# Kernel tuning notes

Hardware: AMD Instinct MI355X
Metric: run time of the kernel (lower is better)

## Reference

```python
import jax, jax.numpy as jnp
import numpy as np

B, L, C = 2, 2048, 1024
H, HD = 16, 64
MAX_SCALE_MUL = float(np.log(100.0))
SCALE = 1.0  # attn_l2_norm=True -> scale is 1


def setup_inputs() -> dict:
    key = jax.random.key(0)
    ks = jax.random.split(key, 6)
    x = jax.random.normal(ks[0], (B, L, C), dtype=jnp.float32)
    attn_bias = jax.random.normal(ks[1], (1, 1, L, L), dtype=jnp.float32)
    w_qkv = jax.random.normal(ks[2], (3 * C, C), dtype=jnp.float32) * (1.0 / np.sqrt(C))
    q_bias = jnp.zeros((C,), dtype=jnp.float32)
    v_bias = jnp.zeros((C,), dtype=jnp.float32)
    scale_mul = jnp.full((1, H, 1, 1), np.log(4.0), dtype=jnp.float32)  # scale_mul_1H11
    w_proj = jax.random.normal(ks[3], (C, C), dtype=jnp.float32) * (1.0 / np.sqrt(C))
    b_proj = jnp.zeros((C,), dtype=jnp.float32)
    return {"x": x, "attn_bias": attn_bias, "w_qkv": w_qkv, "q_bias": q_bias,
            "v_bias": v_bias, "scale_mul": scale_mul, "w_proj": w_proj, "b_proj": b_proj}


def reference(x, attn_bias, w_qkv, q_bias, v_bias, scale_mul, w_proj, b_proj):
    # qkv projection with concatenated bias (q_bias, zeros, v_bias)
    bias = jnp.concatenate([q_bias, jnp.zeros_like(q_bias), v_bias])  # [3C]
    qkv = jnp.einsum('blc,dc->bld', x, w_qkv) + bias                  # [B,L,3C]
    qkv = qkv.reshape(B, L, 3, H, HD).transpose(2, 0, 3, 1, 4)        # [3,B,H,L,HD]
    q, k, v = qkv[0], qkv[1], qkv[2]
    # attn_l2_norm path: L2-normalize q,k; q scaled by exp(clamped scale_mul)
    sm = jnp.exp(jnp.minimum(scale_mul, MAX_SCALE_MUL))               # [1,H,1,1]
    q = q / jnp.linalg.norm(q, axis=-1, keepdims=True) * sm
    k = k / jnp.linalg.norm(k, axis=-1, keepdims=True)
    # slow_attn: scaled scores + bias, softmax, weighted sum
    attn = jnp.einsum('bhld,bhmd->bhlm', q * SCALE, k) + attn_bias    # [B,H,L,L]
    p = jax.nn.softmax(attn, axis=-1)
    oup = jnp.einsum('bhlm,bhmd->bhld', p, v)                         # [B,H,L,HD]
    oup = oup.transpose(0, 2, 1, 3).reshape(B, L, C)
    return jnp.einsum('blc,dc->bld', oup, w_proj) + b_proj
```

## Files before the change

### kernel.cpp

```cpp
#include <hip/hip_runtime.h>
#include <cstdint>
#include <cstddef>
#include <math.h>

typedef __attribute__((ext_vector_type(8))) __bf16 bf16x8;
typedef __attribute__((ext_vector_type(4))) __bf16 bf16x4;
typedef __attribute__((ext_vector_type(4))) float f32x4;
typedef __attribute__((ext_vector_type(4))) unsigned int u32x4;

#define AS1 __attribute__((address_space(1)))
#define AS3 __attribute__((address_space(3)))

#define LOG2E 1.4426950408889634f

__device__ __forceinline__ void gld16(void* lds_uniform, const void* gaddr) {
  __builtin_amdgcn_global_load_lds((const AS1 unsigned int*)gaddr,
                                   (AS3 unsigned int*)lds_uniform, 16, 0, 0);
}

__global__ __launch_bounds__(256)
void prep_kernel(const float* __restrict__ x, const float* __restrict__ wqkv,
                 const float* __restrict__ wproj, const float* __restrict__ bias,
                 __bf16* __restrict__ xb, __bf16* __restrict__ wqkvb,
                 __bf16* __restrict__ wprojb, __bf16* __restrict__ btr) {
  __shared__ __bf16 T[32][264];
  const int b = blockIdx.x;
  const int tid = threadIdx.x;
  if (b < 8192) {
    const float* src; __bf16* dst; int off;
    if (b < 4096)      { src = x;     dst = xb;     off = b; }
    else if (b < 7168) { src = wqkv;  dst = wqkvb;  off = b - 4096; }
    else               { src = wproj; dst = wprojb; off = b - 7168; }
    const int i = (off * 256 + tid) * 4;
    const float4 v = *(const float4*)(src + i);
    bf16x4 o;
    o[0] = (__bf16)v.x; o[1] = (__bf16)v.y; o[2] = (__bf16)v.z; o[3] = (__bf16)v.w;
    *(bf16x4*)(dst + i) = o;
    return;
  }
  const int bb = b - 8192;
  const int rb = bb >> 3, cg = bb & 7;
  const float* src = bias + (size_t)(rb * 32) * 2048 + cg * 256;
#pragma unroll
  for (int i = 0; i < 8; ++i) {
    const int u = i * 256 + tid;
    const int r = u >> 6, c4 = (u & 63) * 4;
    const float4 v = *(const float4*)(src + (size_t)r * 2048 + c4);
    T[r][c4 + 0] = (__bf16)(v.x * LOG2E);
    T[r][c4 + 1] = (__bf16)(v.y * LOG2E);
    T[r][c4 + 2] = (__bf16)(v.z * LOG2E);
    T[r][c4 + 3] = (__bf16)(v.w * LOG2E);
  }
  __syncthreads();
  const int ktl = tid >> 6;
  const int lane = tid & 63, g = lane >> 4, cc = lane & 15;
#pragma unroll
  for (int sub = 0; sub < 2; ++sub) {
    __bf16 outv[16];
#pragma unroll
    for (int v = 0; v < 16; ++v) {
      const int ni = v >> 2, j = v & 3;
      outv[v] = T[sub * 16 + cc][ktl * 64 + ni * 16 + g * 4 + j];
    }
    __bf16* dst = btr + ((size_t)(((rb * 2 + sub) * 32) + cg * 4 + ktl) * 64 + lane) * 16;
    *(bf16x8*)(dst) = *(bf16x8*)(outv);
    *(bf16x8*)(dst + 8) = *(bf16x8*)(outv + 8);
  }
}

__global__ __launch_bounds__(256, 2)
void gemm_qkv_kernel(const __bf16* __restrict__ A, const __bf16* __restrict__ B,
                     const float* __restrict__ q_bias, const float* __restrict__ v_bias,
                     const float* __restrict__ scale_mul,
                     __bf16* __restrict__ qb, __bf16* __restrict__ ktp, __bf16* __restrict__ vb) {
  __shared__ __attribute__((aligned(16))) __bf16 As[2][128 * 32];
  __shared__ __attribute__((aligned(16))) __bf16 Bs[2][128 * 32];
  const int tid = threadIdx.x;
  const int w = tid >> 6, lane = tid & 63;
  const int bid = blockIdx.x;
  const int swz = (bid & 7) * 96 + (bid >> 3);
  const int m0 = (swz / 24) * 128, n0 = (swz % 24) * 128;
  const int wm = (w >> 1) * 64, wn = (w & 1) * 64;
  const int c = lane & 15, g = lane >> 4;
  f32x4 acc[4][4];
#pragma unroll
  for (int i = 0; i < 4; ++i)
#pragma unroll
    for (int j = 0; j < 4; ++j) acc[i][j] = (f32x4)(0.0f);

  const int r_row = lane >> 2;
  const int r_col = (lane & 3) * 16;
  const char* Abase = (const char*)A + (size_t)m0 * 2048;
  const char* Bbase = (const char*)B + (size_t)n0 * 2048;

  for (int kt = 0; kt < 1024; kt += 64) {
#pragma unroll
    for (int ks = 0; ks < 2; ++ks)
#pragma unroll
      for (int s = 0; s < 2; ++s) {
        const int R = w * 2 + s;
        const int row = R * 16 + r_row;
        gld16((char*)&As[ks][0] + R * 1024, Abase + (size_t)row * 2048 + kt * 2 + ks * 64 + r_col);
        gld16((char*)&Bs[ks][0] + R * 1024, Bbase + (size_t)row * 2048 + kt * 2 + ks * 64 + r_col);
      }
    __syncthreads();
#pragma unroll
    for (int ks = 0; ks < 2; ++ks) {
      bf16x8 af[4], bfr[4];
#pragma unroll
      for (int i = 0; i < 4; ++i) {
        af[i]  = *(const bf16x8*)((const char*)&As[ks][0] + (wm + i * 16 + c) * 64 + g * 16);
        bfr[i] = *(const bf16x8*)((const char*)&Bs[ks][0] + (wn + i * 16 + c) * 64 + g * 16);
      }
#pragma unroll
      for (int ni = 0; ni < 4; ++ni)
#pragma unroll
        for (int mi = 0; mi < 4; ++mi)
          acc[ni][mi] = __builtin_amdgcn_mfma_f32_16x16x32_bf16(bfr[ni], af[mi], acc[ni][mi], 0, 0, 0);
    }
    __syncthreads();
  }

  const int nbase = n0 + wn;
  const int which = nbase >> 10;
  const int h = (nbase >> 6) & 15;
  float smh = 1.0f;
  if (which == 0) smh = __expf(fminf(scale_mul[h], 4.605170185988091f)) * LOG2E;
  float4 cb[4];
#pragma unroll
  for (int ni = 0; ni < 4; ++ni) {
    if (which == 0)      cb[ni] = *(const float4*)(q_bias + nbase + ni * 16 + 4 * g);
    else if (which == 2) cb[ni] = *(const float4*)(v_bias + nbase - 2048 + ni * 16 + 4 * g);
    else                 cb[ni] = make_float4(0.f, 0.f, 0.f, 0.f);
  }
  const int mrow0 = m0 + wm;
  const int b2 = mrow0 >> 11;
  const int lpos0 = mrow0 & 2047;
  __bf16* kt_tile = ktp + (size_t)(b2 * 16 + h) * 131072 + (size_t)(lpos0 >> 6) * 4096;
  __bf16* dst_qv = ((which == 0) ? qb : vb) + ((size_t)((b2 * 16 + h) * 2048 + lpos0)) * 64;

#pragma unroll
  for (int mi = 0; mi < 4; ++mi) {
    float v[4][4];
    float ss = 0.0f;
#pragma unroll
    for (int ni = 0; ni < 4; ++ni) {
      v[ni][0] = acc[ni][mi][0] + cb[ni].x;
      v[ni][1] = acc[ni][mi][1] + cb[ni].y;
      v[ni][2] = acc[ni][mi][2] + cb[ni].z;
      v[ni][3] = acc[ni][mi][3] + cb[ni].w;
#pragma unroll
      for (int j = 0; j < 4; ++j) ss += v[ni][j] * v[ni][j];
    }
    ss += __shfl_xor(ss, 16, 64);
    ss += __shfl_xor(ss, 32, 64);
    const float sc = (which == 2) ? 1.0f : (rsqrtf(ss) * smh);
    const int key = mi * 16 + c;
    if (which == 1) {
#pragma unroll
      for (int ni = 0; ni < 4; ++ni) {
        bf16x4 pk;
        pk[0] = (__bf16)(v[ni][0] * sc); pk[1] = (__bf16)(v[ni][1] * sc);
        pk[2] = (__bf16)(v[ni][2] * sc); pk[3] = (__bf16)(v[ni][3] * sc);
        *(bf16x4*)(kt_tile + (ni >> 1) * 2048 + key * 32 + (ni & 1) * 16 + 4 * g) = pk;
      }
    } else {
      __bf16* drow = dst_qv + (size_t)key * 64;
#pragma unroll
      for (int ni = 0; ni < 4; ++ni) {
        bf16x4 pk;
        pk[0] = (__bf16)(v[ni][0] * sc); pk[1] = (__bf16)(v[ni][1] * sc);
        pk[2] = (__bf16)(v[ni][2] * sc); pk[3] = (__bf16)(v[ni][3] * sc);
        *(bf16x4*)(drow + ni * 16 + 4 * g) = pk;
      }
    }
  }
}

__global__ __launch_bounds__(256)
void vtrans_kernel(const __bf16* __restrict__ vb, __bf16* __restrict__ vtp) {
  __shared__ __attribute__((aligned(16))) __bf16 Vs[4][64 * 64];
  const int w = threadIdx.x >> 6, lane = threadIdx.x & 63;
  const int idx = blockIdx.x * 4 + w;
  const int bh = idx >> 5, tile = idx & 31;
  const __bf16* src = vb + ((size_t)bh * 2048 + tile * 64) * 64;
#pragma unroll
  for (int s = 0; s < 8; ++s)
    gld16((char*)&Vs[w][0] + s * 1024, (const char*)src + s * 1024 + lane * 16);
  __syncthreads();
  __bf16* outb = vtp + (size_t)idx * 4096;
  const int gg = lane & 3, cc = lane >> 2;
#pragma unroll
  for (int r = 0; r < 8; ++r) {
    const int o = r * 512 + lane * 8;
    const int ni = r & 3, ks = r >> 2;
    const int hd = ni * 16 + cc;
    const int key0 = ks * 32 + gg * 8;
    bf16x8 pk;
#pragma unroll
    for (int i = 0; i < 8; ++i)
      pk[i] = Vs[w][(key0 + i) * 64 + hd];
    *(bf16x8*)(outb + o) = pk;
  }
}

#define STAGE(t, b) {                                                          \
  const char* _ks = kp + (size_t)(t) * 8192 + w * 1024 + sl16;                 \
  const char* _vs = vp + (size_t)(t) * 8192 + w * 1024 + sl16;                 \
  gld16(&Kb[b][w * 1024], _ks);                                                \
  gld16(&Vb[b][w * 1024], _vs);                                                \
}

#define BAV(ni, j) ((ni * 4 + j < 8) ? bA0[(ni * 4 + j) & 7] : bA1[(ni * 4 + j) & 7])

#define COMPUTE(t, b) {                                                        \
  const char* _bb = bp + (size_t)(t) * 2048 + lane * 32;                       \
  bf16x8 bA0 = *(const bf16x8*)_bb;                                            \
  bf16x8 bA1 = *(const bf16x8*)(_bb + 16);                                     \
  bf16x8 kf[4][2];                                                             \
  _Pragma("unroll")                                                            \
  for (int ni = 0; ni < 4; ++ni)                                               \
    _Pragma("unroll")                                                          \
    for (int ks = 0; ks < 2; ++ks)                                             \
      kf[ni][ks] = *(const bf16x8*)(&Kb[b][0] + ks * 4096 + (ni * 16 + c) * 64 + gsw16); \
  f32x4 sacc[4];                                                               \
  __builtin_amdgcn_s_setprio(1);                                               \
  _Pragma("unroll")                                                            \
  for (int ni = 0; ni < 4; ++ni) {                                             \
    f32x4 s_ = __builtin_amdgcn_mfma_f32_16x16x32_bf16(kf[ni][0], qf[0], (f32x4)(0.0f), 0, 0, 0); \
    sacc[ni] = __builtin_amdgcn_mfma_f32_16x16x32_bf16(kf[ni][1], qf[1], s_, 0, 0, 0); \
  }                                                                            \
  __builtin_amdgcn_s_setprio(0);                                               \
  unsigned qp[4][2];                                                           \
  _Pragma("unroll")                                                            \
  for (int ni = 0; ni < 4; ++ni) {                                             \
    const float p0 = __builtin_amdgcn_exp2f(sacc[ni][0] + (float)BAV(ni, 0));  \
    const float p1 = __builtin_amdgcn_exp2f(sacc[ni][1] + (float)BAV(ni, 1));  \
    const float p2 = __builtin_amdgcn_exp2f(sacc[ni][2] + (float)BAV(ni, 2));  \
    const float p3 = __builtin_amdgcn_exp2f(sacc[ni][3] + (float)BAV(ni, 3));  \
    lsum += (p0 + p1) + (p2 + p3);                                             \
    asm("v_cvt_pk_bf16_f32 %0, %1, %2" : "=v"(qp[ni][0]) : "v"(p0), "v"(p1));  \
    asm("v_cvt_pk_bf16_f32 %0, %1, %2" : "=v"(qp[ni][1]) : "v"(p2), "v"(p3));  \
  }                                                                            \
  bf16x8 pf[2];                                                                \
  _Pragma("unroll")                                                            \
  for (int ks = 0; ks < 2; ++ks) {                                             \
    unsigned x0 = qp[2 * ks][0], x1 = qp[2 * ks][1];                           \
    unsigned y0 = qp[2 * ks + 1][0], y1 = qp[2 * ks + 1][1];                   \
    asm("v_permlane32_swap_b32 %0, %1" : "+v"(x0), "+v"(y0));                  \
    asm("v_permlane16_swap_b32 %0, %1" : "+v"(x0), "+v"(y0));                  \
    asm("v_permlane32_swap_b32 %0, %1" : "+v"(x1), "+v"(y1));                  \
    asm("v_permlane16_swap_b32 %0, %1" : "+v"(x1), "+v"(y1));                  \
    u32x4 t_; t_[0] = x0; t_[1] = x1; t_[2] = y0; t_[3] = y1;                  \
    pf[ks] = __builtin_bit_cast(bf16x8, t_);                                   \
  }                                                                            \
  __builtin_amdgcn_s_setprio(1);                                               \
  _Pragma("unroll")                                                            \
  for (int ni = 0; ni < 4; ++ni) {                                             \
    const bf16x8 v0 = *(const bf16x8*)(&Vb[b][0] + 0 * 4096 + ni * 1024 + c * 64 + gsw16); \
    const bf16x8 v1 = *(const bf16x8*)(&Vb[b][0] + 1 * 4096 + ni * 1024 + c * 64 + gsw16); \
    oacc[ni] = __builtin_amdgcn_mfma_f32_16x16x32_bf16(pf[0], v0, oacc[ni], 0, 0, 0); \
    oacc[ni] = __builtin_amdgcn_mfma_f32_16x16x32_bf16(pf[1], v1, oacc[ni], 0, 0, 0); \
  }                                                                            \
  __builtin_amdgcn_s_setprio(0);                                               \
}

__global__ __launch_bounds__(512, 4)
void attn_kernel(const __bf16* __restrict__ qb, const __bf16* __restrict__ ktp,
                 const __bf16* __restrict__ vtp, const __bf16* __restrict__ btr,
                 __bf16* __restrict__ oupb) {
  __shared__ __attribute__((aligned(16))) char Kb[2][8192];
  __shared__ __attribute__((aligned(16))) char Vb[2][8192];
  const int tid = threadIdx.x, w = tid >> 6, lane = tid & 63;
  const int c = lane & 15, g = lane >> 4;
  const int sl16 = (lane ^ ((lane >> 3) & 3)) * 16;
  const int gsw16 = (g ^ ((c >> 1) & 3)) * 16;
  const int idx = blockIdx.x;
  const int bh = idx & 31, rb = idx >> 5;
  const __bf16* qh = qb + (size_t)bh * (2048 * 64);
  const char* kp = (const char*)ktp + (size_t)bh * (32 * 8192);
  const char* vp = (const char*)vtp + (size_t)bh * (32 * 8192);
  const char* bp = (const char*)btr + (size_t)(rb * 8 + w) * 65536;
  const int q0 = rb * 128 + w * 16;
  const int b2 = bh >> 4, h = bh & 15;

  bf16x8 qf[2];
#pragma unroll
  for (int ks = 0; ks < 2; ++ks)
    qf[ks] = *(const bf16x8*)(qh + (size_t)(q0 + c) * 64 + ks * 32 + g * 8);

  f32x4 oacc[4];
  float lsum = 0.0f;
#pragma unroll
  for (int ni = 0; ni < 4; ++ni) oacc[ni] = (f32x4)(0.0f);

  STAGE(0, 0);
  __syncthreads();
#pragma unroll 1
  for (int tt = 0; tt < 32; tt += 2) {
    if (tt + 1 < 32) STAGE(tt + 1, 1);
    COMPUTE(tt, 0);
    __syncthreads();
    if (tt + 2 < 32) STAGE(tt + 2, 0);
    COMPUTE(tt + 1, 1);
    __syncthreads();
  }

  float l = lsum;
  l += __shfl_xor(l, 16, 64);
  l += __shfl_xor(l, 32, 64);
#pragma unroll
  for (int j = 0; j < 4; ++j) {
    const float lr = __shfl(l, g * 4 + j, 64);
    const float inv = 1.0f / lr;
    const int qrow = q0 + g * 4 + j;
    __bf16* orow = oupb + ((size_t)(b2 * 2048 + qrow) * 16 + h) * 64;
#pragma unroll
    for (int ni = 0; ni < 4; ++ni)
      orow[ni * 16 + c] = (__bf16)(oacc[ni][j] * inv);
  }
}

__global__ __launch_bounds__(256, 2)
void gemm_proj_kernel(const __bf16* __restrict__ A, const __bf16* __restrict__ B,
                      const float* __restrict__ b_proj, float* __restrict__ out) {
  __shared__ __attribute__((aligned(16))) __bf16 As[64 * 32];
  __shared__ __attribute__((aligned(16))) __bf16 Bs[128 * 32];
  const int tid = threadIdx.x;
  const int w = tid >> 6, lane = tid & 63;
  const int c = lane & 15, g = lane >> 4;
  const int m0 = blockIdx.y * 64, n0 = blockIdx.x * 128;
  const int wm = (w >> 1) * 32, wn = (w & 1) * 64;
  f32x4 acc[2][4];
#pragma unroll
  for (int i = 0; i < 2; ++i)
#pragma unroll
    for (int j = 0; j < 4; ++j) acc[i][j] = (f32x4)(0.0f);

  const int r_row = lane >> 2;
  const int r_col = (lane & 3) * 16;
  const char* Abase = (const char*)A + (size_t)m0 * 2048;
  const char* Bbase = (const char*)B + (size_t)n0 * 2048;

  for (int kt = 0; kt < 1024; kt += 32) {
    {
      const int row = w * 16 + r_row;
      gld16((char*)As + w * 1024, Abase + (size_t)row * 2048 + kt * 2 + r_col);
    }
#pragma unroll
    for (int s = 0; s < 2; ++s) {
      const int R = w * 2 + s;
      const int row = R * 16 + r_row;
      gld16((char*)Bs + R * 1024, Bbase + (size_t)row * 2048 + kt * 2 + r_col);
    }
    __syncthreads();
    bf16x8 af[2], bfr[4];
#pragma unroll
    for (int i = 0; i < 2; ++i)
      af[i] = *(const bf16x8*)((const char*)As + (wm + i * 16 + c) * 64 + g * 16);
#pragma unroll
    for (int i = 0; i < 4; ++i)
      bfr[i] = *(const bf16x8*)((const char*)Bs + (wn + i * 16 + c) * 64 + g * 16);
#pragma unroll
    for (int mi = 0; mi < 2; ++mi)
#pragma unroll
      for (int ni = 0; ni < 4; ++ni)
        acc[mi][ni] = __builtin_amdgcn_mfma_f32_16x16x32_bf16(af[mi], bfr[ni], acc[mi][ni], 0, 0, 0);
    __syncthreads();
  }

  float cbias[4];
#pragma unroll
  for (int ni = 0; ni < 4; ++ni) cbias[ni] = b_proj[n0 + wn + ni * 16 + c];
#pragma unroll
  for (int mi = 0; mi < 2; ++mi)
#pragma unroll
    for (int j = 0; j < 4; ++j) {
      const int m = m0 + wm + mi * 16 + g * 4 + j;
      float* orow = out + (size_t)m * 1024 + n0 + wn;
#pragma unroll
      for (int ni = 0; ni < 4; ++ni)
        orow[ni * 16 + c] = acc[mi][ni][j] + cbias[ni];
    }
}

extern "C" void kernel_launch(void* const* d_in, const int* in_sizes, int n_in,
                              void* d_out, int out_size, void* d_ws, size_t ws_size,
                              hipStream_t stream) {
  const float* x         = (const float*)d_in[0];
  const float* attn_bias = (const float*)d_in[1];
  const float* w_qkv     = (const float*)d_in[2];
  const float* q_bias    = (const float*)d_in[3];
  const float* v_bias    = (const float*)d_in[4];
  const float* scale_mul = (const float*)d_in[5];
  const float* w_proj    = (const float*)d_in[6];
  const float* b_proj    = (const float*)d_in[7];
  float* out = (float*)d_out;

  __bf16* xb     = (__bf16*)d_ws;
  __bf16* wqkvb  = xb + 4194304;
  __bf16* wprojb = wqkvb + 3145728;
  __bf16* qb     = wprojb + 1048576;
  __bf16* ktp    = qb + 4194304;
  __bf16* vtp    = ktp + 4194304;
  __bf16* btr    = vtp + 4194304;
  __bf16* vb     = btr + 4194304;
  __bf16* oupb   = xb;

  prep_kernel<<<8704, 256, 0, stream>>>(x, w_qkv, w_proj, attn_bias, xb, wqkvb, wprojb, btr);
  gemm_qkv_kernel<<<768, 256, 0, stream>>>(xb, wqkvb, q_bias, v_bias, scale_mul,
                                           qb, ktp, vb);
  vtrans_kernel<<<256, 256, 0, stream>>>(vb, vtp);
  attn_kernel<<<512, 512, 0, stream>>>(qb, ktp, vtp, btr, oupb);
  gemm_proj_kernel<<<dim3(8, 64), 256, 0, stream>>>(oupb, wprojb, b_proj, out);
}
```

Before: 212.8 us.

## Use 2-wave 128x64 warp tiles in QKV GEMM, deepen proj GEMM K-step

The QKV GEMM now runs 128 threads per block, and each wave computes a full 128x64 output strip with 32 accumulators instead of 64x64. Each B fragment is reused across 8 A fragments, which cuts LDS reads per MFMA. The K-tile layout of the epilogue is recomputed per row to match. The projection GEMM now loads two 32-wide K slices per barrier pair, halving the number of syncs. The trade-off is more register pressure and fewer waves per block in the QKV GEMM, which may reduce latency hiding.

```diff
diff --git a/kernel.cpp b/kernel.cpp
--- a/kernel.cpp
+++ b/kernel.cpp
@@ -68,7 +68,7 @@
   }
 }
 
-__global__ __launch_bounds__(256, 2)
+__global__ __launch_bounds__(128, 2)
 void gemm_qkv_kernel(const __bf16* __restrict__ A, const __bf16* __restrict__ B,
                      const float* __restrict__ q_bias, const float* __restrict__ v_bias,
                      const float* __restrict__ scale_mul,
@@ -80,13 +80,13 @@
   const int bid = blockIdx.x;
   const int swz = (bid & 7) * 96 + (bid >> 3);
   const int m0 = (swz / 24) * 128, n0 = (swz % 24) * 128;
-  const int wm = (w >> 1) * 64, wn = (w & 1) * 64;
+  const int wn = w * 64;
   const int c = lane & 15, g = lane >> 4;
-  f32x4 acc[4][4];
+  f32x4 acc[4][8];
 #pragma unroll
   for (int i = 0; i < 4; ++i)
 #pragma unroll
-    for (int j = 0; j < 4; ++j) acc[i][j] = (f32x4)(0.0f);
+    for (int j = 0; j < 8; ++j) acc[i][j] = (f32x4)(0.0f);
 
   const int r_row = lane >> 2;
   const int r_col = (lane & 3) * 16;
@@ -97,26 +97,26 @@
 #pragma unroll
     for (int ks = 0; ks < 2; ++ks)
 #pragma unroll
-      for (int s = 0; s < 2; ++s) {
-        const int R = w * 2 + s;
-        const int row = R * 16 + r_row;
-        gld16((char*)&As[ks][0] + R * 1024, Abase + (size_t)row * 2048 + kt * 2 + ks * 64 + r_col);
-        gld16((char*)&Bs[ks][0] + R * 1024, Bbase + (size_t)row * 2048 + kt * 2 + ks * 64 + r_col);
+      for (int r = 0; r < 4; ++r) {
+        const int chunk = r * 2 + w;
+        const int row = chunk * 16 + r_row;
+        gld16((char*)&As[ks][0] + chunk * 1024, Abase + (size_t)row * 2048 + kt * 2 + ks * 64 + r_col);
+        gld16((char*)&Bs[ks][0] + chunk * 1024, Bbase + (size_t)row * 2048 + kt * 2 + ks * 64 + r_col);
       }
     __syncthreads();
 #pragma unroll
     for (int ks = 0; ks < 2; ++ks) {
-      bf16x8 af[4], bfr[4];
-#pragma unroll
-      for (int i = 0; i < 4; ++i) {
-        af[i]  = *(const bf16x8*)((const char*)&As[ks][0] + (wm + i * 16 + c) * 64 + g * 16);
+      bf16x8 bfr[4];
+#pragma unroll
+      for (int i = 0; i < 4; ++i)
         bfr[i] = *(const bf16x8*)((const char*)&Bs[ks][0] + (wn + i * 16 + c) * 64 + g * 16);
-      }
-#pragma unroll
-      for (int ni = 0; ni < 4; ++ni)
-#pragma unroll
-        for (int mi = 0; mi < 4; ++mi)
-          acc[ni][mi] = __builtin_amdgcn_mfma_f32_16x16x32_bf16(bfr[ni], af[mi], acc[ni][mi], 0, 0, 0);
+#pragma unroll
+      for (int mi = 0; mi < 8; ++mi) {
+        const bf16x8 af = *(const bf16x8*)((const char*)&As[ks][0] + (mi * 16 + c) * 64 + g * 16);
+#pragma unroll
+        for (int ni = 0; ni < 4; ++ni)
+          acc[ni][mi] = __builtin_amdgcn_mfma_f32_16x16x32_bf16(bfr[ni], af, acc[ni][mi], 0, 0, 0);
+      }
     }
     __syncthreads();
   }
@@ -133,14 +133,13 @@
     else if (which == 2) cb[ni] = *(const float4*)(v_bias + nbase - 2048 + ni * 16 + 4 * g);
     else                 cb[ni] = make_float4(0.f, 0.f, 0.f, 0.f);
   }
-  const int mrow0 = m0 + wm;
-  const int b2 = mrow0 >> 11;
-  const int lpos0 = mrow0 & 2047;
-  __bf16* kt_tile = ktp + (size_t)(b2 * 16 + h) * 131072 + (size_t)(lpos0 >> 6) * 4096;
+  const int b2 = m0 >> 11;
+  const int lpos0 = m0 & 2047;
+  __bf16* kt_head = ktp + (size_t)(b2 * 16 + h) * 131072;
   __bf16* dst_qv = ((which == 0) ? qb : vb) + ((size_t)((b2 * 16 + h) * 2048 + lpos0)) * 64;
 
 #pragma unroll
-  for (int mi = 0; mi < 4; ++mi) {
+  for (int mi = 0; mi < 8; ++mi) {
     float v[4][4];
     float ss = 0.0f;
 #pragma unroll
@@ -157,12 +156,15 @@
     const float sc = (which == 2) ? 1.0f : (rsqrtf(ss) * smh);
     const int key = mi * 16 + c;
     if (which == 1) {
+      const int lpos = lpos0 + key;
+      __bf16* kt_tile = kt_head + (size_t)(lpos >> 6) * 4096;
+      const int k64 = lpos & 63;
 #pragma unroll
       for (int ni = 0; ni < 4; ++ni) {
         bf16x4 pk;
         pk[0] = (__bf16)(v[ni][0] * sc); pk[1] = (__bf16)(v[ni][1] * sc);
         pk[2] = (__bf16)(v[ni][2] * sc); pk[3] = (__bf16)(v[ni][3] * sc);
-        *(bf16x4*)(kt_tile + (ni >> 1) * 2048 + key * 32 + (ni & 1) * 16 + 4 * g) = pk;
+        *(bf16x4*)(kt_tile + (ni >> 1) * 2048 + k64 * 32 + (ni & 1) * 16 + 4 * g) = pk;
       }
     } else {
       __bf16* drow = dst_qv + (size_t)key * 64;
@@ -324,8 +326,8 @@
 __global__ __launch_bounds__(256, 2)
 void gemm_proj_kernel(const __bf16* __restrict__ A, const __bf16* __restrict__ B,
                       const float* __restrict__ b_proj, float* __restrict__ out) {
-  __shared__ __attribute__((aligned(16))) __bf16 As[64 * 32];
-  __shared__ __attribute__((aligned(16))) __bf16 Bs[128 * 32];
+  __shared__ __attribute__((aligned(16))) __bf16 As[2][64 * 32];
+  __shared__ __attribute__((aligned(16))) __bf16 Bs[2][128 * 32];
   const int tid = threadIdx.x;
   const int w = tid >> 6, lane = tid & 63;
   const int c = lane & 15, g = lane >> 4;
@@ -342,30 +344,36 @@
   const char* Abase = (const char*)A + (size_t)m0 * 2048;
   const char* Bbase = (const char*)B + (size_t)n0 * 2048;
 
-  for (int kt = 0; kt < 1024; kt += 32) {
-    {
-      const int row = w * 16 + r_row;
-      gld16((char*)As + w * 1024, Abase + (size_t)row * 2048 + kt * 2 + r_col);
-    }
-#pragma unroll
-    for (int s = 0; s < 2; ++s) {
-      const int R = w * 2 + s;
-      const int row = R * 16 + r_row;
-      gld16((char*)Bs + R * 1024, Bbase + (size_t)row * 2048 + kt * 2 + r_col);
-    }
-    __syncthreads();
-    bf16x8 af[2], bfr[4];
-#pragma unroll
-    for (int i = 0; i < 2; ++i)
-      af[i] = *(const bf16x8*)((const char*)As + (wm + i * 16 + c) * 64 + g * 16);
-#pragma unroll
-    for (int i = 0; i < 4; ++i)
-      bfr[i] = *(const bf16x8*)((const char*)Bs + (wn + i * 16 + c) * 64 + g * 16);
-#pragma unroll
-    for (int mi = 0; mi < 2; ++mi)
-#pragma unroll
-      for (int ni = 0; ni < 4; ++ni)
-        acc[mi][ni] = __builtin_amdgcn_mfma_f32_16x16x32_bf16(af[mi], bfr[ni], acc[mi][ni], 0, 0, 0);
+  for (int kt = 0; kt < 1024; kt += 64) {
+#pragma unroll
+    for (int ks = 0; ks < 2; ++ks) {
+      {
+        const int row = w * 16 + r_row;
+        gld16((char*)&As[ks][0] + w * 1024, Abase + (size_t)row * 2048 + kt * 2 + ks * 64 + r_col);
+      }
+#pragma unroll
+      for (int s = 0; s < 2; ++s) {
+        const int R = w * 2 + s;
+        const int row = R * 16 + r_row;
+        gld16((char*)&Bs[ks][0] + R * 1024, Bbase + (size_t)row * 2048 + kt * 2 + ks * 64 + r_col);
+      }
+    }
+    __syncthreads();
+#pragma unroll
+    for (int ks = 0; ks < 2; ++ks) {
+      bf16x8 af[2], bfr[4];
+#pragma unroll
+      for (int i = 0; i < 2; ++i)
+        af[i] = *(const bf16x8*)((const char*)&As[ks][0] + (wm + i * 16 + c) * 64 + g * 16);
+#pragma unroll
+      for (int i = 0; i < 4; ++i)
+        bfr[i] = *(const bf16x8*)((const char*)&Bs[ks][0] + (wn + i * 16 + c) * 64 + g * 16);
+#pragma unroll
+      for (int mi = 0; mi < 2; ++mi)
+#pragma unroll
+        for (int ni = 0; ni < 4; ++ni)
+          acc[mi][ni] = __builtin_amdgcn_mfma_f32_16x16x32_bf16(af[mi], bfr[ni], acc[mi][ni], 0, 0, 0);
+    }
     __syncthreads();
   }
 
@@ -408,7 +416,7 @@
   __bf16* oupb   = xb;
 
   prep_kernel<<<8704, 256, 0, stream>>>(x, w_qkv, w_proj, attn_bias, xb, wqkvb, wprojb, btr);
-  gemm_qkv_kernel<<<768, 256, 0, stream>>>(xb, wqkvb, q_bias, v_bias, scale_mul,
+  gemm_qkv_kernel<<<768, 128, 0, stream>>>(xb, wqkvb, q_bias, v_bias, scale_mul,
                                            qb, ktp, vb);
   vtrans_kernel<<<256, 256, 0, stream>>>(vb, vtp);
   attn_kernel<<<512, 512, 0, stream>>>(qb, ktp, vtp, btr, oupb);
```

Result: no change. 212.3 us (-0.2%).

## Fuse V transpose into QKV GEMM epilogue, widen prep and proj K-steps

Applied to the files above, without the earlier changes.

The QKV GEMM epilogue now writes V straight into the transposed tile layout the attention kernel expects, which removes the separate vtrans kernel launch and its round trip of V through global memory. The fp32-to-bf16 prep kernel now has each block convert four chunks, cutting the block count. The projection GEMM loads two K-slices per iteration so it needs half as many barriers. The cost is that the V epilogue uses scattered 2-byte stores, which may coalesce poorly.

```diff
diff --git a/kernel.cpp b/kernel.cpp
--- a/kernel.cpp
+++ b/kernel.cpp
@@ -26,19 +26,22 @@
   __shared__ __bf16 T[32][264];
   const int b = blockIdx.x;
   const int tid = threadIdx.x;
-  if (b < 8192) {
-    const float* src; __bf16* dst; int off;
-    if (b < 4096)      { src = x;     dst = xb;     off = b; }
-    else if (b < 7168) { src = wqkv;  dst = wqkvb;  off = b - 4096; }
-    else               { src = wproj; dst = wprojb; off = b - 7168; }
-    const int i = (off * 256 + tid) * 4;
-    const float4 v = *(const float4*)(src + i);
-    bf16x4 o;
-    o[0] = (__bf16)v.x; o[1] = (__bf16)v.y; o[2] = (__bf16)v.z; o[3] = (__bf16)v.w;
-    *(bf16x4*)(dst + i) = o;
+  if (b < 2048) {
+    const float* src; __bf16* dst; int fb;
+    if (b < 1024)      { src = x;     dst = xb;     fb = b; }
+    else if (b < 1792) { src = wqkv;  dst = wqkvb;  fb = b - 1024; }
+    else               { src = wproj; dst = wprojb; fb = b - 1792; }
+#pragma unroll
+    for (int q = 0; q < 4; ++q) {
+      const size_t i = ((size_t)fb * 1024 + q * 256 + tid) * 4;
+      const float4 v = *(const float4*)(src + i);
+      bf16x4 o;
+      o[0] = (__bf16)v.x; o[1] = (__bf16)v.y; o[2] = (__bf16)v.z; o[3] = (__bf16)v.w;
+      *(bf16x4*)(dst + i) = o;
+    }
     return;
   }
-  const int bb = b - 8192;
+  const int bb = b - 2048;
   const int rb = bb >> 3, cg = bb & 7;
   const float* src = bias + (size_t)(rb * 32) * 2048 + cg * 256;
 #pragma unroll
@@ -72,7 +75,7 @@
 void gemm_qkv_kernel(const __bf16* __restrict__ A, const __bf16* __restrict__ B,
                      const float* __restrict__ q_bias, const float* __restrict__ v_bias,
                      const float* __restrict__ scale_mul,
-                     __bf16* __restrict__ qb, __bf16* __restrict__ ktp, __bf16* __restrict__ vb) {
+                     __bf16* __restrict__ qb, __bf16* __restrict__ ktp, __bf16* __restrict__ vtp) {
   __shared__ __attribute__((aligned(16))) __bf16 As[2][128 * 32];
   __shared__ __attribute__((aligned(16))) __bf16 Bs[2][128 * 32];
   const int tid = threadIdx.x;
@@ -137,7 +140,8 @@
   const int b2 = mrow0 >> 11;
   const int lpos0 = mrow0 & 2047;
   __bf16* kt_tile = ktp + (size_t)(b2 * 16 + h) * 131072 + (size_t)(lpos0 >> 6) * 4096;
-  __bf16* dst_qv = ((which == 0) ? qb : vb) + ((size_t)((b2 * 16 + h) * 2048 + lpos0)) * 64;
+  __bf16* dst_q = qb + ((size_t)((b2 * 16 + h) * 2048 + lpos0)) * 64;
+  __bf16* vtile = vtp + ((size_t)((b2 * 16 + h) * 32) + (lpos0 >> 6)) * 4096;
 
 #pragma unroll
   for (int mi = 0; mi < 4; ++mi) {
@@ -164,8 +168,8 @@
         pk[2] = (__bf16)(v[ni][2] * sc); pk[3] = (__bf16)(v[ni][3] * sc);
         *(bf16x4*)(kt_tile + (ni >> 1) * 2048 + key * 32 + (ni & 1) * 16 + 4 * g) = pk;
       }
-    } else {
-      __bf16* drow = dst_qv + (size_t)key * 64;
+    } else if (which == 0) {
+      __bf16* drow = dst_q + (size_t)key * 64;
 #pragma unroll
       for (int ni = 0; ni < 4; ++ni) {
         bf16x4 pk;
@@ -173,34 +177,17 @@
         pk[2] = (__bf16)(v[ni][2] * sc); pk[3] = (__bf16)(v[ni][3] * sc);
         *(bf16x4*)(drow + ni * 16 + 4 * g) = pk;
       }
-    }
-  }
-}
-
-__global__ __launch_bounds__(256)
-void vtrans_kernel(const __bf16* __restrict__ vb, __bf16* __restrict__ vtp) {
-  __shared__ __attribute__((aligned(16))) __bf16 Vs[4][64 * 64];
-  const int w = threadIdx.x >> 6, lane = threadIdx.x & 63;
-  const int idx = blockIdx.x * 4 + w;
-  const int bh = idx >> 5, tile = idx & 31;
-  const __bf16* src = vb + ((size_t)bh * 2048 + tile * 64) * 64;
-#pragma unroll
-  for (int s = 0; s < 8; ++s)
-    gld16((char*)&Vs[w][0] + s * 1024, (const char*)src + s * 1024 + lane * 16);
-  __syncthreads();
-  __bf16* outb = vtp + (size_t)idx * 4096;
-  const int gg = lane & 3, cc = lane >> 2;
-#pragma unroll
-  for (int r = 0; r < 8; ++r) {
-    const int o = r * 512 + lane * 8;
-    const int ni = r & 3, ks = r >> 2;
-    const int hd = ni * 16 + cc;
-    const int key0 = ks * 32 + gg * 8;
-    bf16x8 pk;
-#pragma unroll
-    for (int i = 0; i < 8; ++i)
-      pk[i] = Vs[w][(key0 + i) * 64 + hd];
-    *(bf16x8*)(outb + o) = pk;
+    } else {
+      const int ks2 = mi >> 1;
+      const int gg  = ((mi & 1) << 1) | (c >> 3);
+      const int e   = c & 7;
+      __bf16* basep = vtile + ks2 * 2048 + gg * 8 + e;
+#pragma unroll
+      for (int ni = 0; ni < 4; ++ni)
+#pragma unroll
+        for (int j = 0; j < 4; ++j)
+          basep[ni * 512 + (4 * g + j) * 32] = (__bf16)v[ni][j];
+    }
   }
 }
 
@@ -324,8 +311,8 @@
 __global__ __launch_bounds__(256, 2)
 void gemm_proj_kernel(const __bf16* __restrict__ A, const __bf16* __restrict__ B,
                       const float* __restrict__ b_proj, float* __restrict__ out) {
-  __shared__ __attribute__((aligned(16))) __bf16 As[64 * 32];
-  __shared__ __attribute__((aligned(16))) __bf16 Bs[128 * 32];
+  __shared__ __attribute__((aligned(16))) __bf16 As[2][64 * 32];
+  __shared__ __attribute__((aligned(16))) __bf16 Bs[2][128 * 32];
   const int tid = threadIdx.x;
   const int w = tid >> 6, lane = tid & 63;
   const int c = lane & 15, g = lane >> 4;
@@ -342,30 +329,36 @@
   const char* Abase = (const char*)A + (size_t)m0 * 2048;
   const char* Bbase = (const char*)B + (size_t)n0 * 2048;
 
-  for (int kt = 0; kt < 1024; kt += 32) {
-    {
-      const int row = w * 16 + r_row;
-      gld16((char*)As + w * 1024, Abase + (size_t)row * 2048 + kt * 2 + r_col);
-    }
-#pragma unroll
-    for (int s = 0; s < 2; ++s) {
-      const int R = w * 2 + s;
-      const int row = R * 16 + r_row;
-      gld16((char*)Bs + R * 1024, Bbase + (size_t)row * 2048 + kt * 2 + r_col);
-    }
-    __syncthreads();
-    bf16x8 af[2], bfr[4];
-#pragma unroll
-    for (int i = 0; i < 2; ++i)
-      af[i] = *(const bf16x8*)((const char*)As + (wm + i * 16 + c) * 64 + g * 16);
-#pragma unroll
-    for (int i = 0; i < 4; ++i)
-      bfr[i] = *(const bf16x8*)((const char*)Bs + (wn + i * 16 + c) * 64 + g * 16);
-#pragma unroll
-    for (int mi = 0; mi < 2; ++mi)
-#pragma unroll
-      for (int ni = 0; ni < 4; ++ni)
-        acc[mi][ni] = __builtin_amdgcn_mfma_f32_16x16x32_bf16(af[mi], bfr[ni], acc[mi][ni], 0, 0, 0);
+  for (int kt = 0; kt < 1024; kt += 64) {
+#pragma unroll
+    for (int ks = 0; ks < 2; ++ks) {
+      {
+        const int row = w * 16 + r_row;
+        gld16((char*)&As[ks][0] + w * 1024, Abase + (size_t)row * 2048 + kt * 2 + ks * 64 + r_col);
+      }
+#pragma unroll
+      for (int s = 0; s < 2; ++s) {
+        const int R = w * 2 + s;
+        const int row = R * 16 + r_row;
+        gld16((char*)&Bs[ks][0] + R * 1024, Bbase + (size_t)row * 2048 + kt * 2 + ks * 64 + r_col);
+      }
+    }
+    __syncthreads();
+#pragma unroll
+    for (int ks = 0; ks < 2; ++ks) {
+      bf16x8 af[2], bfr[4];
+#pragma unroll
+      for (int i = 0; i < 2; ++i)
+        af[i] = *(const bf16x8*)((const char*)&As[ks][0] + (wm + i * 16 + c) * 64 + g * 16);
+#pragma unroll
+      for (int i = 0; i < 4; ++i)
+        bfr[i] = *(const bf16x8*)((const char*)&Bs[ks][0] + (wn + i * 16 + c) * 64 + g * 16);
+#pragma unroll
+      for (int mi = 0; mi < 2; ++mi)
+#pragma unroll
+        for (int ni = 0; ni < 4; ++ni)
+          acc[mi][ni] = __builtin_amdgcn_mfma_f32_16x16x32_bf16(af[mi], bfr[ni], acc[mi][ni], 0, 0, 0);
+    }
     __syncthreads();
   }
 
@@ -404,13 +397,11 @@
   __bf16* ktp    = qb + 4194304;
   __bf16* vtp    = ktp + 4194304;
   __bf16* btr    = vtp + 4194304;
-  __bf16* vb     = btr + 4194304;
   __bf16* oupb   = xb;
 
-  prep_kernel<<<8704, 256, 0, stream>>>(x, w_qkv, w_proj, attn_bias, xb, wqkvb, wprojb, btr);
+  prep_kernel<<<2560, 256, 0, stream>>>(x, w_qkv, w_proj, attn_bias, xb, wqkvb, wprojb, btr);
   gemm_qkv_kernel<<<768, 256, 0, stream>>>(xb, wqkvb, q_bias, v_bias, scale_mul,
-                                           qb, ktp, vb);
-  vtrans_kernel<<<256, 256, 0, stream>>>(vb, vtp);
+                                           qb, ktp, vtp);
   attn_kernel<<<512, 512, 0, stream>>>(qb, ktp, vtp, btr, oupb);
   gemm_proj_kernel<<<dim3(8, 64), 256, 0, stream>>>(oupb, wprojb, b_proj, out);
 }
```

Result: faster. 205.5 us (-3.4%).
